# Optimization experiments

Hardware: AMD Instinct MI355X
Metric: run time of the kernel (lower is better)

Reference implementation:

```python
import jax, jax.numpy as jnp
import numpy as np

DIM = 512
HID = 1536          # int(2*(4*512)/3) rounded up to multiple of 256
N_EXPERTS = 8
TOP_K = 2
SHARED_HID = HID * 2  # n_shared_experts scales hidden dim of the single shared MLP
B, S = 4, 2048


def _swiglu(x, w1, w3, w2):
    return (jax.nn.silu(x @ w1.T) * (x @ w3.T)) @ w2.T


def setup_inputs() -> dict:
    key = jax.random.key(0)
    ks = jax.random.split(key, 8)
    sc_d = 1.0 / np.sqrt(DIM)
    sc_h = 1.0 / np.sqrt(HID)
    sc_sh = 1.0 / np.sqrt(SHARED_HID)
    return {
        "x": jax.random.normal(ks[0], (B, S, DIM), jnp.float32),
        "gate_w": jax.random.normal(ks[1], (N_EXPERTS, DIM), jnp.float32) * sc_d,
        "w1": jax.random.normal(ks[2], (N_EXPERTS, HID, DIM), jnp.float32) * sc_d,
        "w3": jax.random.normal(ks[3], (N_EXPERTS, HID, DIM), jnp.float32) * sc_d,
        "w2": jax.random.normal(ks[4], (N_EXPERTS, DIM, HID), jnp.float32) * sc_h,
        "sw1": jax.random.normal(ks[5], (SHARED_HID, DIM), jnp.float32) * sc_d,
        "sw3": jax.random.normal(ks[6], (SHARED_HID, DIM), jnp.float32) * sc_d,
        "sw2": jax.random.normal(ks[7], (DIM, SHARED_HID), jnp.float32) * sc_sh,
    }


def reference(x, gate_w, w1, w3, w2, sw1, sw3, sw2):
    b, s, d = x.shape
    t = b * s
    xf = x.reshape(t, d)

    # --- gate (greedy top-k over softmax scores, fp32) ---
    logits = xf.astype(jnp.float32) @ gate_w.astype(jnp.float32).T  # [T, E]
    scores = jax.nn.softmax(logits, axis=-1)
    topk_w, topk_i = jax.lax.top_k(scores, TOP_K)                    # [T, K]

    # per-token combine weight for each expert: sum of topk weights routed to it
    e = gate_w.shape[0]
    comb = jnp.zeros((t, e), jnp.float32).at[jnp.arange(t)[:, None], topk_i].add(topk_w)

    # --- routed experts: weighted sum of SwiGLU outputs ---
    y = jnp.zeros((t, d), x.dtype)
    for i in range(e):  # fixed small number of structurally distinct experts
        ye = _swiglu(xf, w1[i], w3[i], w2[i]).astype(x.dtype)
        y = y + comb[:, i:i + 1].astype(x.dtype) * ye
    y = y.reshape(b, s, d)

    # --- shared expert added to all tokens ---
    shared = _swiglu(xf, sw1, sw3, sw2).reshape(b, s, d).astype(x.dtype)
    return y + shared
```

## Files before the change

kernel.cpp:

```cpp
#include <hip/hip_runtime.h>

#define T_TOK 8192
#define DIMSZ 512
#define HIDSZ 1536
#define SHIDSZ 3072
#define NE 8

typedef __attribute__((ext_vector_type(4))) float f32x4;
typedef __attribute__((ext_vector_type(8))) short s16x8;

__device__ __forceinline__ unsigned short f2bf(float f) {
  unsigned int u = __float_as_uint(f);
  u += 0x7fff + ((u >> 16) & 1);
  return (unsigned short)(u >> 16);
}

__device__ __forceinline__ void async16(void* lds, const void* g) {
  __builtin_amdgcn_global_load_lds((const __attribute__((address_space(1))) void*)g,
                                   (__attribute__((address_space(3))) void*)lds,
                                   16, 0, 0);
}

__global__ void cvt_bf16(const float* __restrict__ s, unsigned short* __restrict__ d, int n4) {
  int i = blockIdx.x * blockDim.x + threadIdx.x;
  if (i < n4) {
    float4 v = ((const float4*)s)[i];
    ushort4 o;
    o.x = f2bf(v.x); o.y = f2bf(v.y); o.z = f2bf(v.z); o.w = f2bf(v.w);
    ((ushort4*)d)[i] = o;
  }
}

#define GATE_BLOCKS 256
#define GATE_TPB (T_TOK / GATE_BLOCKS)
#define GATE_TPW (GATE_TPB / 4)

__global__ __launch_bounds__(256) void gate_kernel(
    const float* __restrict__ x, const float* __restrict__ gw,
    float* __restrict__ tw, int* __restrict__ ti, int* __restrict__ cnt) {
  __shared__ int lcnt[NE];
  const int tid = threadIdx.x;
  if (tid < NE) lcnt[tid] = 0;
  __syncthreads();
  const int w = tid >> 6, l = tid & 63;

  float gv[NE][8];
  const float* gbase = gw + l * 8;
#pragma unroll
  for (int e = 0; e < NE; ++e)
#pragma unroll
    for (int j = 0; j < 8; ++j) gv[e][j] = gbase[e * DIMSZ + j];

  const int tok0 = blockIdx.x * GATE_TPB + w * GATE_TPW;
  for (int it = 0; it < GATE_TPW; ++it) {
    const int t = tok0 + it;
    const float* xr = x + (size_t)t * DIMSZ + l * 8;
    float xv[8];
#pragma unroll
    for (int j = 0; j < 8; ++j) xv[j] = xr[j];
    float p[NE];
#pragma unroll
    for (int e = 0; e < NE; ++e) {
      float s = 0.f;
#pragma unroll
      for (int j = 0; j < 8; ++j) s = fmaf(xv[j], gv[e][j], s);
      p[e] = s;
    }
#pragma unroll
    for (int e = 0; e < NE; ++e) {
      float v = p[e];
#pragma unroll
      for (int off = 32; off > 0; off >>= 1) v += __shfl_xor(v, off);
      p[e] = v;
    }
    float m = p[0];
#pragma unroll
    for (int e = 1; e < NE; ++e) m = fmaxf(m, p[e]);
    float ex[NE], s = 0.f;
#pragma unroll
    for (int e = 0; e < NE; ++e) { ex[e] = __expf(p[e] - m); s += ex[e]; }
    float inv = 1.f / s;
    int e0 = 0; float v0 = p[0];
#pragma unroll
    for (int e = 1; e < NE; ++e) if (p[e] > v0) { v0 = p[e]; e0 = e; }
    int e1 = -1; float v1 = -3.4e38f;
#pragma unroll
    for (int e = 0; e < NE; ++e) if (e != e0 && p[e] > v1) { v1 = p[e]; e1 = e; }
    if (l == 0) {
      ti[2 * t] = e0;     tw[2 * t] = ex[e0] * inv;
      ti[2 * t + 1] = e1; tw[2 * t + 1] = ex[e1] * inv;
      atomicAdd(&lcnt[e0], 1);
      atomicAdd(&lcnt[e1], 1);
    }
  }
  __syncthreads();
  if (tid < NE) atomicAdd(&cnt[tid], lcnt[tid]);
}

__global__ void scan_kernel(const int* __restrict__ cnt, int* __restrict__ base,
                            int* __restrict__ cursor) {
  if (threadIdx.x == 0 && blockIdx.x == 0) {
    int r = 0;
    for (int e = 0; e < NE; ++e) { base[e] = r; cursor[e] = r; r += cnt[e]; }
  }
}

__global__ __launch_bounds__(256) void scatter_kernel(
    const int* __restrict__ ti, int* __restrict__ cursor,
    int* __restrict__ tok, int* __restrict__ dst) {
  __shared__ int lcnt[NE], gbase[NE];
  const int tid = threadIdx.x;
  if (tid < NE) lcnt[tid] = 0;
  __syncthreads();
  const int t = blockIdx.x * 256 + tid;
  const int e0 = ti[2 * t], e1 = ti[2 * t + 1];
  const int p0 = atomicAdd(&lcnt[e0], 1);
  const int p1 = atomicAdd(&lcnt[e1], 1);
  __syncthreads();
  if (tid < NE) gbase[tid] = atomicAdd(&cursor[tid], lcnt[tid]);
  __syncthreads();
  const int i0 = gbase[e0] + p0, i1 = gbase[e1] + p1;
  tok[i0] = t; dst[i0] = 2 * t;
  tok[i1] = t; dst[i1] = 2 * t + 1;
}

__global__ __launch_bounds__(256, 3) void gemm1_all(
    const unsigned short* __restrict__ xb, const int* __restrict__ tok,
    const unsigned short* __restrict__ w1b, const unsigned short* __restrict__ w3b,
    const unsigned short* __restrict__ sw1b, const unsigned short* __restrict__ sw3b,
    unsigned short* __restrict__ g_rt, unsigned short* __restrict__ g_sh,
    const int* __restrict__ cnt, const int* __restrict__ base) {
  const int bx = blockIdx.x;
  const int e = bx >> 6, mt = bx & 63;
  const int n0 = blockIdx.y * 64;
  int cntE, rowbase, N;
  const unsigned short *B1, *B3;
  unsigned short* G;
  bool indirect;
  if (e < NE) {
    N = HIDSZ;
    if (n0 >= HIDSZ) return;
    cntE = cnt[e];
    if (mt * 128 >= cntE) return;
    rowbase = base[e];
    B1 = w1b + (size_t)e * HIDSZ * DIMSZ + (size_t)n0 * DIMSZ;
    B3 = w3b + (size_t)e * HIDSZ * DIMSZ + (size_t)n0 * DIMSZ;
    G = g_rt + (size_t)rowbase * HIDSZ;
    indirect = true;
  } else {
    N = SHIDSZ; cntE = T_TOK; rowbase = 0;
    B1 = sw1b + (size_t)n0 * DIMSZ;
    B3 = sw3b + (size_t)n0 * DIMSZ;
    G = g_sh;
    indirect = false;
  }
  const int m0 = mt * 128;

  __shared__ __align__(16) unsigned short As[128 * 64];
  __shared__ __align__(16) unsigned short B1s[64 * 64];
  __shared__ __align__(16) unsigned short B3s[64 * 64];

  const int tid = threadIdx.x;
  const int w = tid >> 6, lane = tid & 63;
  const int wr = w >> 1, wc = w & 1;
  const int lhi = lane >> 4, llo = lane & 15;

  const unsigned short* aSrc[4];
  int aDst[4];
#pragma unroll
  for (int i = 0; i < 4; ++i) {
    int L = i * 256 + tid, row = L >> 3, c = L & 7, sc = c ^ (row & 7);
    int ar = min(m0 + row, cntE - 1);
    int rowg = indirect ? tok[rowbase + ar] : ar;
    aSrc[i] = xb + (size_t)rowg * DIMSZ + sc * 8;
    aDst[i] = (i * 256 + (tid & ~63)) * 8;
  }
  const unsigned short *b1Src[2], *b3Src[2];
  int bDst[2];
#pragma unroll
  for (int i = 0; i < 2; ++i) {
    int L = i * 256 + tid, row = L >> 3, c = L & 7, sc = c ^ (row & 7);
    b1Src[i] = B1 + (size_t)row * DIMSZ + sc * 8;
    b3Src[i] = B3 + (size_t)row * DIMSZ + sc * 8;
    bDst[i] = (i * 256 + (tid & ~63)) * 8;
  }

  int aOff[4][2], bOff[2][2];
#pragma unroll
  for (int m = 0; m < 4; ++m) {
    int r = wr * 64 + m * 16 + llo;
#pragma unroll
    for (int s = 0; s < 2; ++s)
      aOff[m][s] = r * 64 + (((lhi + 4 * s) ^ (r & 7)) * 8);
  }
#pragma unroll
  for (int n = 0; n < 2; ++n) {
    int r = wc * 32 + n * 16 + llo;
#pragma unroll
    for (int s = 0; s < 2; ++s)
      bOff[n][s] = r * 64 + (((lhi + 4 * s) ^ (r & 7)) * 8);
  }

  f32x4 acc1[4][2], acc3[4][2];
#pragma unroll
  for (int m = 0; m < 4; ++m)
#pragma unroll
    for (int n = 0; n < 2; ++n) {
      acc1[m][n] = f32x4{0.f, 0.f, 0.f, 0.f};
      acc3[m][n] = f32x4{0.f, 0.f, 0.f, 0.f};
    }

  for (int k0 = 0; k0 < DIMSZ; k0 += 64) {
#pragma unroll
    for (int i = 0; i < 4; ++i) async16(&As[aDst[i]], aSrc[i] + k0);
#pragma unroll
    for (int i = 0; i < 2; ++i) {
      async16(&B1s[bDst[i]], b1Src[i] + k0);
      async16(&B3s[bDst[i]], b3Src[i] + k0);
    }
    __syncthreads();
#pragma unroll
    for (int s = 0; s < 2; ++s) {
      s16x8 a[4], b1f[2], b3f[2];
#pragma unroll
      for (int m = 0; m < 4; ++m) a[m] = *(const s16x8*)&As[aOff[m][s]];
#pragma unroll
      for (int n = 0; n < 2; ++n) {
        b1f[n] = *(const s16x8*)&B1s[bOff[n][s]];
        b3f[n] = *(const s16x8*)&B3s[bOff[n][s]];
      }
#pragma unroll
      for (int m = 0; m < 4; ++m)
#pragma unroll
        for (int n = 0; n < 2; ++n) {
          acc1[m][n] = __builtin_amdgcn_mfma_f32_16x16x32_bf16(a[m], b1f[n], acc1[m][n], 0, 0, 0);
          acc3[m][n] = __builtin_amdgcn_mfma_f32_16x16x32_bf16(a[m], b3f[n], acc3[m][n], 0, 0, 0);
        }
    }
    __syncthreads();
  }

#pragma unroll
  for (int m = 0; m < 4; ++m)
#pragma unroll
    for (int n = 0; n < 2; ++n)
#pragma unroll
      for (int q = 0; q < 4; ++q) {
        int r = wr * 64 + m * 16 + lhi * 4 + q;
        if (m0 + r < cntE) {
          float h1 = acc1[m][n][q], h3 = acc3[m][n][q];
          float val = (h1 / (1.f + __expf(-h1))) * h3;
          G[(size_t)(m0 + r) * N + n0 + wc * 32 + n * 16 + llo] = f2bf(val);
        }
      }
}

__global__ __launch_bounds__(256, 3) void gemm2_all(
    const unsigned short* __restrict__ g_rt, const unsigned short* __restrict__ g_sh,
    const unsigned short* __restrict__ w2b, const unsigned short* __restrict__ sw2b,
    const int* __restrict__ cnt, const int* __restrict__ base,
    const int* __restrict__ dst, const float* __restrict__ tw,
    float* __restrict__ out) {
  const int bx = blockIdx.x;
  const int e = bx >> 7, mt = bx & 127;
  const int n0 = blockIdx.y * 128;
  int cntE, rowbase, K;
  const unsigned short *A, *B;
  bool routed;
  if (e < NE) {
    cntE = cnt[e];
    if (mt * 64 >= cntE) return;
    rowbase = base[e];
    A = g_rt + (size_t)rowbase * HIDSZ;
    B = w2b + (size_t)e * DIMSZ * HIDSZ + (size_t)n0 * HIDSZ;
    K = HIDSZ;
    routed = true;
  } else {
    cntE = T_TOK; rowbase = 0;
    A = g_sh;
    B = sw2b + (size_t)n0 * SHIDSZ;
    K = SHIDSZ;
    routed = false;
  }
  const int m0 = mt * 64;

  __shared__ __align__(16) unsigned short As[2 * 64 * 64];
  __shared__ __align__(16) unsigned short Bs[2 * 128 * 64];

  const int tid = threadIdx.x;
  const int w = tid >> 6, lane = tid & 63;
  const int wr = w >> 1, wc = w & 1;
  const int lhi = lane >> 4, llo = lane & 15;

  const unsigned short* aSrc[2];
  int aDst[2];
#pragma unroll
  for (int i = 0; i < 2; ++i) {
    int L = i * 256 + tid, row = L >> 3, c = L & 7, sc = c ^ (row & 7);
    int ar = min(m0 + row, cntE - 1);
    aSrc[i] = A + (size_t)ar * K + sc * 8;
    aDst[i] = (i * 256 + (tid & ~63)) * 8;
  }
  const unsigned short* bSrc[4];
  int bDst[4];
#pragma unroll
  for (int i = 0; i < 4; ++i) {
    int L = i * 256 + tid, row = L >> 3, c = L & 7, sc = c ^ (row & 7);
    bSrc[i] = B + (size_t)row * K + sc * 8;
    bDst[i] = (i * 256 + (tid & ~63)) * 8;
  }

  int aOff[2][2], bOff[4][2];
#pragma unroll
  for (int m = 0; m < 2; ++m) {
    int r = wr * 32 + m * 16 + llo;
#pragma unroll
    for (int s = 0; s < 2; ++s)
      aOff[m][s] = r * 64 + (((lhi + 4 * s) ^ (r & 7)) * 8);
  }
#pragma unroll
  for (int n = 0; n < 4; ++n) {
    int r = wc * 64 + n * 16 + llo;
#pragma unroll
    for (int s = 0; s < 2; ++s)
      bOff[n][s] = r * 64 + (((lhi + 4 * s) ^ (r & 7)) * 8);
  }

  f32x4 acc[2][4];
#pragma unroll
  for (int i = 0; i < 2; ++i)
#pragma unroll
    for (int j = 0; j < 4; ++j) acc[i][j] = f32x4{0.f, 0.f, 0.f, 0.f};

  const int nt = K >> 6;
  int cur = 0;
#pragma unroll
  for (int i = 0; i < 2; ++i) async16(&As[aDst[i]], aSrc[i]);
#pragma unroll
  for (int i = 0; i < 4; ++i) async16(&Bs[bDst[i]], bSrc[i]);

  for (int t = 0; t < nt; ++t) {
    const bool more = (t + 1) < nt;
    if (more) {
      const int k1 = (t + 1) << 6;
      const int nxtA = (cur ^ 1) * 4096, nxtB = (cur ^ 1) * 8192;
#pragma unroll
      for (int i = 0; i < 2; ++i) async16(&As[nxtA + aDst[i]], aSrc[i] + k1);
#pragma unroll
      for (int i = 0; i < 4; ++i) async16(&Bs[nxtB + bDst[i]], bSrc[i] + k1);
      asm volatile("s_waitcnt vmcnt(6)" ::: "memory");
    } else {
      asm volatile("s_waitcnt vmcnt(0)" ::: "memory");
    }
    __builtin_amdgcn_s_barrier();
    const int cA = cur * 4096, cB = cur * 8192;
#pragma unroll
    for (int s = 0; s < 2; ++s) {
      s16x8 a[2], b[4];
#pragma unroll
      for (int m = 0; m < 2; ++m) a[m] = *(const s16x8*)&As[cA + aOff[m][s]];
#pragma unroll
      for (int n = 0; n < 4; ++n) b[n] = *(const s16x8*)&Bs[cB + bOff[n][s]];
#pragma unroll
      for (int i = 0; i < 2; ++i)
#pragma unroll
        for (int j = 0; j < 4; ++j)
          acc[i][j] = __builtin_amdgcn_mfma_f32_16x16x32_bf16(a[i], b[j], acc[i][j], 0, 0, 0);
    }
    if (more) { __builtin_amdgcn_s_barrier(); cur ^= 1; }
  }

#pragma unroll
  for (int i = 0; i < 2; ++i)
#pragma unroll
    for (int q = 0; q < 4; ++q) {
      int r = wr * 32 + i * 16 + lhi * 4 + q;
      if (m0 + r < cntE) {
        int orow; float wgt;
        if (routed) {
          int d = dst[rowbase + m0 + r];
          orow = d >> 1;
          wgt = tw[d];
        } else {
          orow = m0 + r;
          wgt = 1.f;
        }
        float* orow_p = out + (size_t)orow * DIMSZ + n0 + wc * 64 + llo;
#pragma unroll
        for (int j = 0; j < 4; ++j)
          atomicAdd(&orow_p[j * 16], wgt * acc[i][j][q]);
      }
    }
}

extern "C" void kernel_launch(void* const* d_in, const int* in_sizes, int n_in,
                              void* d_out, int out_size, void* d_ws, size_t ws_size,
                              hipStream_t stream) {
  const float* x   = (const float*)d_in[0];
  const float* gw  = (const float*)d_in[1];
  const float* w1  = (const float*)d_in[2];
  const float* w3  = (const float*)d_in[3];
  const float* w2  = (const float*)d_in[4];
  const float* sw1 = (const float*)d_in[5];
  const float* sw3 = (const float*)d_in[6];
  const float* sw2 = (const float*)d_in[7];
  float* out = (float*)d_out;

  char* p = (char*)d_ws;
  auto alloc = [&](size_t bytes) {
    char* r = p;
    p += (bytes + 255) & ~(size_t)255;
    return r;
  };
  unsigned short* xb   = (unsigned short*)alloc((size_t)T_TOK * DIMSZ * 2);
  unsigned short* w1b  = (unsigned short*)alloc((size_t)NE * HIDSZ * DIMSZ * 2);
  unsigned short* w3b  = (unsigned short*)alloc((size_t)NE * HIDSZ * DIMSZ * 2);
  unsigned short* w2b  = (unsigned short*)alloc((size_t)NE * DIMSZ * HIDSZ * 2);
  unsigned short* sw1b = (unsigned short*)alloc((size_t)SHIDSZ * DIMSZ * 2);
  unsigned short* sw3b = (unsigned short*)alloc((size_t)SHIDSZ * DIMSZ * 2);
  unsigned short* sw2b = (unsigned short*)alloc((size_t)DIMSZ * SHIDSZ * 2);
  unsigned short* g_rt = (unsigned short*)alloc((size_t)2 * T_TOK * HIDSZ * 2);
  unsigned short* g_sh = (unsigned short*)alloc((size_t)T_TOK * SHIDSZ * 2);
  float* tw = (float*)alloc((size_t)2 * T_TOK * 4);
  int* ti   = (int*)alloc((size_t)2 * T_TOK * 4);
  int* tok  = (int*)alloc((size_t)2 * T_TOK * 4);
  int* dst  = (int*)alloc((size_t)2 * T_TOK * 4);
  int* meta = (int*)alloc(256);
  int* cnt = meta, *cursor = meta + 8, *base = meta + 16;

  auto cvt = [&](const float* s, unsigned short* d, size_t n) {
    int n4 = (int)(n / 4);
    cvt_bf16<<<(n4 + 255) / 256, 256, 0, stream>>>(s, d, n4);
  };
  cvt(x, xb, (size_t)T_TOK * DIMSZ);
  cvt(w1, w1b, (size_t)NE * HIDSZ * DIMSZ);
  cvt(w3, w3b, (size_t)NE * HIDSZ * DIMSZ);
  cvt(w2, w2b, (size_t)NE * DIMSZ * HIDSZ);
  cvt(sw1, sw1b, (size_t)SHIDSZ * DIMSZ);
  cvt(sw3, sw3b, (size_t)SHIDSZ * DIMSZ);
  cvt(sw2, sw2b, (size_t)DIMSZ * SHIDSZ);

  hipMemsetAsync(meta, 0, 64, stream);
  hipMemsetAsync(out, 0, (size_t)T_TOK * DIMSZ * 4, stream);
  gate_kernel<<<GATE_BLOCKS, 256, 0, stream>>>(x, gw, tw, ti, cnt);
  scan_kernel<<<1, 64, 0, stream>>>(cnt, base, cursor);
  scatter_kernel<<<T_TOK / 256, 256, 0, stream>>>(ti, cursor, tok, dst);

  gemm1_all<<<dim3((NE + 1) * (T_TOK / 128), SHIDSZ / 64), 256, 0, stream>>>(
      xb, tok, w1b, w3b, sw1b, sw3b, g_rt, g_sh, cnt, base);

  gemm2_all<<<dim3(NE * (T_TOK / 64) + (T_TOK / 64), DIMSZ / 128), 256, 0, stream>>>(
      g_rt, g_sh, w2b, sw2b, cnt, base, dst, tw, out);
}
```

Baseline: 429.9 us.

## Split gemm2 into shared store pass and routed atomic pass; remap block order

The second GEMM is split into two kernels. The shared-expert kernel writes its output with plain stores, which initialises the output buffer, so the memset is dropped. The routed kernel then atomically adds the weighted expert outputs on top of it. Block indices in gemm1 and both gemm2 kernels are remapped so that tiles are interleaved across expert groups (8-way stride), which is meant to spread the work across XCDs and improve L2 locality. This removes a full output memset and half the atomics, at the cost of one extra launch and a strict ordering dependency between the two kernels.

```diff
diff --git a/kernel.cpp b/kernel.cpp
--- a/kernel.cpp
+++ b/kernel.cpp
@@ -130,7 +130,7 @@
     const unsigned short* __restrict__ sw1b, const unsigned short* __restrict__ sw3b,
     unsigned short* __restrict__ g_rt, unsigned short* __restrict__ g_sh,
     const int* __restrict__ cnt, const int* __restrict__ base) {
-  const int bx = blockIdx.x;
+  const int bx = (blockIdx.x & 7) * 72 + (blockIdx.x >> 3);
   const int e = bx >> 6, mt = bx & 63;
   const int n0 = blockIdx.y * 64;
   int cntE, rowbase, N;
@@ -255,35 +255,12 @@
       }
 }
 
-__global__ __launch_bounds__(256, 3) void gemm2_all(
-    const unsigned short* __restrict__ g_rt, const unsigned short* __restrict__ g_sh,
-    const unsigned short* __restrict__ w2b, const unsigned short* __restrict__ sw2b,
-    const int* __restrict__ cnt, const int* __restrict__ base,
+template <bool ROUTED>
+__device__ __forceinline__ void gemm2_core(
+    const unsigned short* __restrict__ A, const unsigned short* __restrict__ B,
+    int K, int cntE, int m0, int n0, int rowbase,
     const int* __restrict__ dst, const float* __restrict__ tw,
     float* __restrict__ out) {
-  const int bx = blockIdx.x;
-  const int e = bx >> 7, mt = bx & 127;
-  const int n0 = blockIdx.y * 128;
-  int cntE, rowbase, K;
-  const unsigned short *A, *B;
-  bool routed;
-  if (e < NE) {
-    cntE = cnt[e];
-    if (mt * 64 >= cntE) return;
-    rowbase = base[e];
-    A = g_rt + (size_t)rowbase * HIDSZ;
-    B = w2b + (size_t)e * DIMSZ * HIDSZ + (size_t)n0 * HIDSZ;
-    K = HIDSZ;
-    routed = true;
-  } else {
-    cntE = T_TOK; rowbase = 0;
-    A = g_sh;
-    B = sw2b + (size_t)n0 * SHIDSZ;
-    K = SHIDSZ;
-    routed = false;
-  }
-  const int m0 = mt * 64;
-
   __shared__ __align__(16) unsigned short As[2 * 64 * 64];
   __shared__ __align__(16) unsigned short Bs[2 * 128 * 64];
 
@@ -376,21 +353,48 @@
     for (int q = 0; q < 4; ++q) {
       int r = wr * 32 + i * 16 + lhi * 4 + q;
       if (m0 + r < cntE) {
-        int orow; float wgt;
-        if (routed) {
+        if constexpr (ROUTED) {
           int d = dst[rowbase + m0 + r];
-          orow = d >> 1;
-          wgt = tw[d];
+          int orow = d >> 1;
+          float wgt = tw[d];
+          float* orow_p = out + (size_t)orow * DIMSZ + n0 + wc * 64 + llo;
+#pragma unroll
+          for (int j = 0; j < 4; ++j)
+            atomicAdd(&orow_p[j * 16], wgt * acc[i][j][q]);
         } else {
-          orow = m0 + r;
-          wgt = 1.f;
+          int orow = m0 + r;
+          float* orow_p = out + (size_t)orow * DIMSZ + n0 + wc * 64 + llo;
+#pragma unroll
+          for (int j = 0; j < 4; ++j)
+            orow_p[j * 16] = acc[i][j][q];
         }
-        float* orow_p = out + (size_t)orow * DIMSZ + n0 + wc * 64 + llo;
-#pragma unroll
-        for (int j = 0; j < 4; ++j)
-          atomicAdd(&orow_p[j * 16], wgt * acc[i][j][q]);
       }
     }
+}
+
+__global__ __launch_bounds__(256, 3) void gemm2_shared(
+    const unsigned short* __restrict__ g_sh, const unsigned short* __restrict__ sw2b,
+    float* __restrict__ out) {
+  const int mt = (blockIdx.x & 7) * 16 + (blockIdx.x >> 3);
+  const int n0 = blockIdx.y * 128;
+  gemm2_core<false>(g_sh, sw2b + (size_t)n0 * SHIDSZ, SHIDSZ, T_TOK,
+                    mt * 64, n0, 0, nullptr, nullptr, out);
+}
+
+__global__ __launch_bounds__(256, 3) void gemm2_routed(
+    const unsigned short* __restrict__ g_rt, const unsigned short* __restrict__ w2b,
+    const int* __restrict__ cnt, const int* __restrict__ base,
+    const int* __restrict__ dst, const float* __restrict__ tw,
+    float* __restrict__ out) {
+  const int bx = (blockIdx.x & 7) * 128 + (blockIdx.x >> 3);
+  const int e = bx >> 7, mt = bx & 127;
+  const int cntE = cnt[e];
+  if (mt * 64 >= cntE) return;
+  const int rowbase = base[e];
+  const int n0 = blockIdx.y * 128;
+  gemm2_core<true>(g_rt + (size_t)rowbase * HIDSZ,
+                   w2b + (size_t)e * DIMSZ * HIDSZ + (size_t)n0 * HIDSZ,
+                   HIDSZ, cntE, mt * 64, n0, rowbase, dst, tw, out);
 }
 
 extern "C" void kernel_launch(void* const* d_in, const int* in_sizes, int n_in,
@@ -441,7 +445,6 @@
   cvt(sw2, sw2b, (size_t)DIMSZ * SHIDSZ);
 
   hipMemsetAsync(meta, 0, 64, stream);
-  hipMemsetAsync(out, 0, (size_t)T_TOK * DIMSZ * 4, stream);
   gate_kernel<<<GATE_BLOCKS, 256, 0, stream>>>(x, gw, tw, ti, cnt);
   scan_kernel<<<1, 64, 0, stream>>>(cnt, base, cursor);
   scatter_kernel<<<T_TOK / 256, 256, 0, stream>>>(ti, cursor, tok, dst);
@@ -449,6 +452,7 @@
   gemm1_all<<<dim3((NE + 1) * (T_TOK / 128), SHIDSZ / 64), 256, 0, stream>>>(
       xb, tok, w1b, w3b, sw1b, sw3b, g_rt, g_sh, cnt, base);
 
-  gemm2_all<<<dim3(NE * (T_TOK / 64) + (T_TOK / 64), DIMSZ / 128), 256, 0, stream>>>(
-      g_rt, g_sh, w2b, sw2b, cnt, base, dst, tw, out);
-}
+  gemm2_shared<<<dim3(T_TOK / 64, DIMSZ / 128), 256, 0, stream>>>(g_sh, sw2b, out);
+  gemm2_routed<<<dim3(NE * (T_TOK / 64), DIMSZ / 128), 256, 0, stream>>>(
+      g_rt, w2b, cnt, base, dst, tw, out);
+}
```

New measurement: 647.8 us. +50.7%, slower.
